# Performance work log

Hardware: AMD Instinct MI355X
Metric: run time of the kernel (lower is better)

## Reference

```python
import jax, jax.numpy as jnp
import numpy as np

B, E, H = 16384, 1024, 1024  # batch, input_size(=delta_size=mask_size), hidden_size


def setup_inputs() -> dict:
    key = jax.random.key(0)
    ks = jax.random.split(key, 16)
    stdv = 1.0 / np.sqrt(H)
    u = lambda k, shape: jax.random.uniform(k, shape, jnp.float32, -stdv, stdv)
    return {
        "x": jax.random.normal(ks[0], (B, E), jnp.float32),
        "x_mask": (jax.random.uniform(ks[1], (B, E)) < 0.5).astype(jnp.float32),
        "delta": jax.random.uniform(ks[2], (B, E), jnp.float32),
        "x_last_observed": jax.random.normal(ks[3], (B, E), jnp.float32),
        "x_mean": jax.random.normal(ks[4], (B, E), jnp.float32),
        "hs": jax.random.normal(ks[5], (B, H), jnp.float32),
        # gamma decay linears (delta_size -> delta_size), torch Linear convention y = x @ W.T + b
        "gx_w": u(ks[6], (E, E)), "gx_b": u(ks[7], (E,)),
        "gh_w": u(ks[8], (E, E)), "gh_b": u(ks[9], (E,)),
        # GRU cell (input 2E -> hidden H), gates ordered [r, z, n]
        "w_ih": u(ks[10], (2 * E, 3 * H)), "b_ih": u(ks[11], (3 * H,)),
        "w_hh": u(ks[12], (H, 3 * H)), "b_hh": u(ks[13], (3 * H,)),
    }


def reference(x, x_mask, delta, x_last_observed, x_mean, hs,
              gx_w, gx_b, gh_w, gh_b, w_ih, w_hh, b_ih, b_hh):
    # decay gates: exp(-max(0, Linear(delta)))
    delta_x = jnp.exp(-jax.nn.relu(delta @ gx_w.T + gx_b))  # [B, E]
    delta_h = jnp.exp(-jax.nn.relu(delta @ gh_w.T + gh_b))  # [B, H] (E == H)
    # masked blend of observed / decayed-last / mean
    x_t = x_mask * x + (1.0 - x_mask) * (delta_x * x_last_observed + (1.0 - delta_x) * x_mean)
    h = delta_h * hs
    inputs = jnp.concatenate([x_t, x_mask], axis=-1)  # [B, 2E]
    gi = inputs @ w_ih + b_ih                         # [B, 3H]
    gh = h @ w_hh + b_hh                              # [B, 3H]
    i_r, i_z, i_n = jnp.split(gi, 3, axis=-1)
    h_r, h_z, h_n = jnp.split(gh, 3, axis=-1)
    r = jax.nn.sigmoid(i_r + h_r)
    z = jax.nn.sigmoid(i_z + h_z)
    n = jnp.tanh(i_n + r * h_n)
    return (1.0 - z) * n + z * h
```

## Files before the change

### kernel.cpp

```cpp
#include <hip/hip_runtime.h>
#include <hip/hip_bf16.h>
#include <stdint.h>


#define Bn 16384
#define En 1024
#define Hn 1024

typedef __bf16 bf16x8 __attribute__((ext_vector_type(8)));
typedef float f32x4 __attribute__((ext_vector_type(4)));
typedef unsigned short u16x8 __attribute__((ext_vector_type(8)));

__device__ __forceinline__ void gload_lds16(const void* g, void* l) {
  __builtin_amdgcn_global_load_lds(
      (const __attribute__((address_space(1))) void*)g,
      (__attribute__((address_space(3))) void*)l, 16, 0, 0);
}

__device__ __forceinline__ unsigned short f2bf(float f) {
  __hip_bfloat16 h = __float2bfloat16(f);
  return __builtin_bit_cast(unsigned short, h);
}


__global__ void conv_f32_bf16(const float* __restrict__ in,
                              unsigned short* __restrict__ out, long n) {
  long stride = (long)gridDim.x * blockDim.x;
  for (long i = (long)blockIdx.x * blockDim.x + threadIdx.x; i * 8 < n; i += stride) {
    long b = i * 8;
    float4 a0 = *(const float4*)&in[b];
    float4 a1 = *(const float4*)&in[b + 4];
    u16x8 o;
    o[0] = f2bf(a0.x); o[1] = f2bf(a0.y); o[2] = f2bf(a0.z); o[3] = f2bf(a0.w);
    o[4] = f2bf(a1.x); o[5] = f2bf(a1.y); o[6] = f2bf(a1.z); o[7] = f2bf(a1.w);
    *(u16x8*)&out[b] = o;
  }
}

__global__ void conv_mask_k(const float* __restrict__ in,
                            unsigned short* __restrict__ U) {
  long n = (long)Bn * En;
  long stride = (long)gridDim.x * blockDim.x;
  for (long i = (long)blockIdx.x * blockDim.x + threadIdx.x; i * 8 < n; i += stride) {
    long b = i * 8;
    long row = b >> 10;
    int col = (int)(b & 1023);
    float4 a0 = *(const float4*)&in[b];
    float4 a1 = *(const float4*)&in[b + 4];
    u16x8 o;
    o[0] = f2bf(a0.x); o[1] = f2bf(a0.y); o[2] = f2bf(a0.z); o[3] = f2bf(a0.w);
    o[4] = f2bf(a1.x); o[5] = f2bf(a1.y); o[6] = f2bf(a1.z); o[7] = f2bf(a1.w);
    *(u16x8*)&U[row * 2048 + 1024 + col] = o;
  }
}

__global__ void transpose_conv(const float* __restrict__ in,
                               unsigned short* __restrict__ out, int R, int C) {
  __shared__ float tile[32][33];
  int bc = blockIdx.x * 32, br = blockIdx.y * 32;
  int tx = threadIdx.x, ty = threadIdx.y;
#pragma unroll
  for (int i = 0; i < 32; i += 8)
    tile[ty + i][tx] = in[(size_t)(br + ty + i) * C + (bc + tx)];
  __syncthreads();
#pragma unroll
  for (int i = 0; i < 32; i += 8)
    out[(size_t)(bc + ty + i) * R + (br + tx)] = f2bf(tile[tx][ty + i]);
}


template <int EPI>
__launch_bounds__(256)
__global__ void gemm_nt(const unsigned short* __restrict__ A,
                        const unsigned short* __restrict__ Bt,
                        int M, int N, int K,
                        const float* __restrict__ bias,
                        const float* __restrict__ e0, const float* __restrict__ e1,
                        const float* __restrict__ e2, const float* __restrict__ e3,
                        unsigned short* __restrict__ ob, float* __restrict__ of,
                        int ldo) {
  __shared__ unsigned short sA[128 * 32];
  __shared__ unsigned short sB[128 * 32];
  const int t = threadIdx.x;
  const int lane = t & 63;
  const int w = t >> 6;
  const int wr = w >> 1, wc = w & 1;
  const int rowA0 = blockIdx.x * 128, colB0 = blockIdx.y * 128;

  f32x4 acc[4][4] = {};

  const int fe0 = t * 8;
  const int r0 = fe0 >> 5, c0 = fe0 & 31;
  const int fe1 = (t + 256) * 8;
  const int r1 = fe1 >> 5, c1 = fe1 & 31;

  const unsigned short* Ab0 = A + (size_t)(rowA0 + r0) * K + c0;
  const unsigned short* Ab1 = A + (size_t)(rowA0 + r1) * K + c1;
  const unsigned short* Bb0 = Bt + (size_t)(colB0 + r0) * K + c0;
  const unsigned short* Bb1 = Bt + (size_t)(colB0 + r1) * K + c1;
  unsigned short* sA0 = &sA[t * 8];
  unsigned short* sA1 = &sA[(t + 256) * 8];
  unsigned short* sB0 = &sB[t * 8];
  unsigned short* sB1 = &sB[(t + 256) * 8];

  const int arow = lane & 15;
  const int kh = (lane >> 4) * 8;

  for (int k0 = 0; k0 < K; k0 += 32) {
    gload_lds16(Ab0 + k0, sA0);
    gload_lds16(Ab1 + k0, sA1);
    gload_lds16(Bb0 + k0, sB0);
    gload_lds16(Bb1 + k0, sB1);
    __syncthreads();
    bf16x8 af[4], bfr[4];
#pragma unroll
    for (int m = 0; m < 4; ++m)
      af[m] = *(const bf16x8*)&sA[(wr * 64 + m * 16 + arow) * 32 + kh];
#pragma unroll
    for (int n = 0; n < 4; ++n)
      bfr[n] = *(const bf16x8*)&sB[(wc * 64 + n * 16 + arow) * 32 + kh];
#pragma unroll
    for (int m = 0; m < 4; ++m)
#pragma unroll
      for (int n = 0; n < 4; ++n)
        acc[m][n] = __builtin_amdgcn_mfma_f32_16x16x32_bf16(af[m], bfr[n], acc[m][n], 0, 0, 0);
    __syncthreads();
  }

  const int crow0 = (lane >> 4) * 4;
  const int ccol = lane & 15;
#pragma unroll
  for (int m = 0; m < 4; ++m) {
#pragma unroll
    for (int n = 0; n < 4; ++n) {
#pragma unroll
      for (int j = 0; j < 4; ++j) {
        const int row = rowA0 + wr * 64 + m * 16 + crow0 + j;
        const int col = colB0 + wc * 64 + n * 16 + ccol;
        float v = acc[m][n][j];
        if constexpr (EPI == 0) {
          float dx = expf(-fmaxf(v + bias[col], 0.f));
          size_t idx = (size_t)row * 1024 + col;
          float xv = e0[idx], mv = e1[idx], xl = e2[idx], xm = e3[idx];
          float xt = mv * xv + (1.f - mv) * (dx * xl + (1.f - dx) * xm);
          ob[(size_t)row * ldo + col] = f2bf(xt);
        } else if constexpr (EPI == 1) {
          float dh = expf(-fmaxf(v + bias[col], 0.f));
          float hv = dh * e0[(size_t)row * 1024 + col];
          ob[(size_t)row * ldo + col] = f2bf(hv);
          of[(size_t)row * ldo + col] = hv;
        } else {
          of[(size_t)row * (size_t)ldo + col] = v;
        }
      }
    }
  }
}

__device__ __forceinline__ float sigm(float x) { return 1.f / (1.f + expf(-x)); }

__global__ void gates_k(const float* __restrict__ Gi, const float* __restrict__ Gh,
                        const float* Hf, const float* __restrict__ b_ih,
                        const float* __restrict__ b_hh, float* out,
                        int rows) {
  long n4 = (long)rows * Hn / 4;
  long stride = (long)gridDim.x * blockDim.x;
  for (long i4 = (long)blockIdx.x * blockDim.x + threadIdx.x; i4 < n4; i4 += stride) {
    long i = i4 * 4;
    long row = i >> 10;
    int col = (int)(i & 1023);
    const float* gi = Gi + row * 3072 + col;
    const float* gh = Gh + row * 3072 + col;
    float4 ir = *(const float4*)(gi);
    float4 iz = *(const float4*)(gi + 1024);
    float4 in_ = *(const float4*)(gi + 2048);
    float4 hr = *(const float4*)(gh);
    float4 hz = *(const float4*)(gh + 1024);
    float4 hn = *(const float4*)(gh + 2048);
    float4 bir = *(const float4*)&b_ih[col];
    float4 biz = *(const float4*)&b_ih[1024 + col];
    float4 bin_ = *(const float4*)&b_ih[2048 + col];
    float4 bhr = *(const float4*)&b_hh[col];
    float4 bhz = *(const float4*)&b_hh[1024 + col];
    float4 bhn = *(const float4*)&b_hh[2048 + col];
    float4 hv = *(const float4*)&Hf[i];
    float4 o;
#pragma unroll
    for (int c = 0; c < 4; ++c) {
      float r0 = sigm(((const float*)&ir)[c] + ((const float*)&bir)[c] +
                      ((const float*)&hr)[c] + ((const float*)&bhr)[c]);
      float z0 = sigm(((const float*)&iz)[c] + ((const float*)&biz)[c] +
                      ((const float*)&hz)[c] + ((const float*)&bhz)[c]);
      float nn = tanhf(((const float*)&in_)[c] + ((const float*)&bin_)[c] +
                       r0 * (((const float*)&hn)[c] + ((const float*)&bhn)[c]));
      ((float*)&o)[c] = (1.f - z0) * nn + z0 * ((const float*)&hv)[c];
    }
    *(float4*)&out[i] = o;
  }
}


extern "C" void kernel_launch(void* const* d_in, const int* in_sizes, int n_in,
                              void* d_out, int out_size, void* d_ws, size_t ws_size,
                              hipStream_t stream) {
  const float* x     = (const float*)d_in[0];
  const float* xmask = (const float*)d_in[1];
  const float* delta = (const float*)d_in[2];
  const float* xlast = (const float*)d_in[3];
  const float* xmean = (const float*)d_in[4];
  const float* hs    = (const float*)d_in[5];
  const float* gx_w  = (const float*)d_in[6];
  const float* gx_b  = (const float*)d_in[7];
  const float* gh_w  = (const float*)d_in[8];
  const float* gh_b  = (const float*)d_in[9];
  const float* w_ih  = (const float*)d_in[10];
  const float* b_ih  = (const float*)d_in[11];
  const float* w_hh  = (const float*)d_in[12];
  const float* b_hh  = (const float*)d_in[13];
  float* out = (float*)d_out;

  char* ws = (char*)d_ws;
  size_t off = 0;
  auto alloc = [&](size_t bytes) {
    char* p = ws + off;
    off += (bytes + 255) & ~(size_t)255;
    return p;
  };
  unsigned short* delta_bf = (unsigned short*)alloc((size_t)Bn * En * 2);
  unsigned short* U        = (unsigned short*)alloc((size_t)Bn * 2 * En * 2);
  unsigned short* Hbf      = (unsigned short*)alloc((size_t)Bn * Hn * 2);
  unsigned short* gxw_bf   = (unsigned short*)alloc((size_t)En * En * 2);
  unsigned short* ghw_bf   = (unsigned short*)alloc((size_t)En * En * 2);
  unsigned short* wihT     = (unsigned short*)alloc((size_t)3 * Hn * 2 * En * 2);
  unsigned short* whhT     = (unsigned short*)alloc((size_t)3 * Hn * Hn * 2);
  float*          Hf32     = out;

  int nchunk = 64;
  for (int c = 4; c <= 64; c *= 2) {
    size_t need = off + 2ull * (Bn / c) * 3 * Hn * 4 + 512;
    if (need <= ws_size) { nchunk = c; break; }
  }
  const int CROWS = Bn / nchunk;
  float* GiC = (float*)alloc((size_t)CROWS * 3 * Hn * 4);
  float* GhC = (float*)alloc((size_t)CROWS * 3 * Hn * 4);

  conv_f32_bf16<<<2048, 256, 0, stream>>>(delta, delta_bf, (long)Bn * En);
  conv_f32_bf16<<<512, 256, 0, stream>>>(gx_w, gxw_bf, (long)En * En);
  conv_f32_bf16<<<512, 256, 0, stream>>>(gh_w, ghw_bf, (long)En * En);
  conv_mask_k<<<2048, 256, 0, stream>>>(xmask, U);
  transpose_conv<<<dim3(3 * Hn / 32, 2 * En / 32), dim3(32, 8), 0, stream>>>(w_ih, wihT, 2 * En, 3 * Hn);
  transpose_conv<<<dim3(3 * Hn / 32, Hn / 32), dim3(32, 8), 0, stream>>>(w_hh, whhT, Hn, 3 * Hn);

  gemm_nt<0><<<dim3(Bn / 128, En / 128), 256, 0, stream>>>(
      delta_bf, gxw_bf, Bn, En, En, gx_b, x, xmask, xlast, xmean, U, nullptr, 2 * En);
  gemm_nt<1><<<dim3(Bn / 128, Hn / 128), 256, 0, stream>>>(
      delta_bf, ghw_bf, Bn, Hn, En, gh_b, hs, nullptr, nullptr, nullptr, Hbf, Hf32, Hn);

  for (int c = 0; c < nchunk; ++c) {
    const unsigned short* Uc = U + (size_t)c * CROWS * 2 * En;
    const unsigned short* Hc = Hbf + (size_t)c * CROWS * Hn;
    const float* Hfc = Hf32 + (size_t)c * CROWS * Hn;
    float* outc = out + (size_t)c * CROWS * Hn;
    gemm_nt<2><<<dim3(CROWS / 128, 3 * Hn / 128), 256, 0, stream>>>(
        Uc, wihT, CROWS, 3 * Hn, 2 * En, nullptr, nullptr, nullptr, nullptr, nullptr,
        nullptr, GiC, 3 * Hn);
    gemm_nt<2><<<dim3(CROWS / 128, 3 * Hn / 128), 256, 0, stream>>>(
        Hc, whhT, CROWS, 3 * Hn, Hn, nullptr, nullptr, nullptr, nullptr, nullptr,
        nullptr, GhC, 3 * Hn);
    gates_k<<<2048, 256, 0, stream>>>(GiC, GhC, Hfc, b_ih, b_hh, outc, CROWS);
  }
}
```

Before: 1.149 ms.

## Stage GEMM epilogue through LDS for vectorized stores and remap blocks per XCD

The GEMM epilogue now writes each wave's accumulator fragment to a shared-memory staging buffer, then reads it back row-contiguously so bias, auxiliary inputs and outputs use float4 and 4-wide bf16 accesses instead of scalar strided ones. The 2D grid is also flattened to 1D and remapped so consecutive tiles land on the same XCD, which should improve L2 reuse of A/B tiles. The cost is extra LDS (about 19KB per block), which may lower occupancy, plus some index arithmetic.

```diff
diff --git a/kernel.cpp b/kernel.cpp
--- a/kernel.cpp
+++ b/kernel.cpp
@@ -10,6 +10,7 @@
 typedef __bf16 bf16x8 __attribute__((ext_vector_type(8)));
 typedef float f32x4 __attribute__((ext_vector_type(4)));
 typedef unsigned short u16x8 __attribute__((ext_vector_type(8)));
+typedef unsigned short u16x4 __attribute__((ext_vector_type(4)));
 
 __device__ __forceinline__ void gload_lds16(const void* g, void* l) {
   __builtin_amdgcn_global_load_lds(
@@ -73,7 +74,7 @@
 __launch_bounds__(256)
 __global__ void gemm_nt(const unsigned short* __restrict__ A,
                         const unsigned short* __restrict__ Bt,
-                        int M, int N, int K,
+                        int gridX, int gridY, int K,
                         const float* __restrict__ bias,
                         const float* __restrict__ e0, const float* __restrict__ e1,
                         const float* __restrict__ e2, const float* __restrict__ e3,
@@ -81,23 +82,32 @@
                         int ldo) {
   __shared__ unsigned short sA[128 * 32];
   __shared__ unsigned short sB[128 * 32];
+  __shared__ float sEpi[4][16][76];
+
+  const int nwg = gridX * gridY;
+  const int q = nwg >> 3, r = nwg & 7;
+  const int xcd = (int)blockIdx.x & 7, pos = (int)blockIdx.x >> 3;
+  const int wg = (xcd < r ? xcd * (q + 1) : r * (q + 1) + (xcd - r) * q) + pos;
+  const int by = wg / gridX;
+  const int bx = wg - by * gridX;
+
   const int t = threadIdx.x;
   const int lane = t & 63;
   const int w = t >> 6;
   const int wr = w >> 1, wc = w & 1;
-  const int rowA0 = blockIdx.x * 128, colB0 = blockIdx.y * 128;
+  const int rowA0 = bx * 128, colB0 = by * 128;
 
   f32x4 acc[4][4] = {};
 
   const int fe0 = t * 8;
-  const int r0 = fe0 >> 5, c0 = fe0 & 31;
+  const int r0 = fe0 >> 5, c0e = fe0 & 31;
   const int fe1 = (t + 256) * 8;
-  const int r1 = fe1 >> 5, c1 = fe1 & 31;
-
-  const unsigned short* Ab0 = A + (size_t)(rowA0 + r0) * K + c0;
-  const unsigned short* Ab1 = A + (size_t)(rowA0 + r1) * K + c1;
-  const unsigned short* Bb0 = Bt + (size_t)(colB0 + r0) * K + c0;
-  const unsigned short* Bb1 = Bt + (size_t)(colB0 + r1) * K + c1;
+  const int r1 = fe1 >> 5, c1e = fe1 & 31;
+
+  const unsigned short* Ab0 = A + (size_t)(rowA0 + r0) * K + c0e;
+  const unsigned short* Ab1 = A + (size_t)(rowA0 + r1) * K + c1e;
+  const unsigned short* Bb0 = Bt + (size_t)(colB0 + r0) * K + c0e;
+  const unsigned short* Bb1 = Bt + (size_t)(colB0 + r1) * K + c1e;
   unsigned short* sA0 = &sA[t * 8];
   unsigned short* sA1 = &sA[(t + 256) * 8];
   unsigned short* sB0 = &sB[t * 8];
@@ -127,31 +137,59 @@
     __syncthreads();
   }
 
+  const int ccol = lane & 15;
   const int crow0 = (lane >> 4) * 4;
-  const int ccol = lane & 15;
+  const int rr0 = lane >> 4;
+  const int cc0 = (lane & 15) * 4;
+
 #pragma unroll
   for (int m = 0; m < 4; ++m) {
 #pragma unroll
-    for (int n = 0; n < 4; ++n) {
-#pragma unroll
-      for (int j = 0; j < 4; ++j) {
-        const int row = rowA0 + wr * 64 + m * 16 + crow0 + j;
-        const int col = colB0 + wc * 64 + n * 16 + ccol;
-        float v = acc[m][n][j];
-        if constexpr (EPI == 0) {
-          float dx = expf(-fmaxf(v + bias[col], 0.f));
-          size_t idx = (size_t)row * 1024 + col;
-          float xv = e0[idx], mv = e1[idx], xl = e2[idx], xm = e3[idx];
-          float xt = mv * xv + (1.f - mv) * (dx * xl + (1.f - dx) * xm);
-          ob[(size_t)row * ldo + col] = f2bf(xt);
-        } else if constexpr (EPI == 1) {
-          float dh = expf(-fmaxf(v + bias[col], 0.f));
-          float hv = dh * e0[(size_t)row * 1024 + col];
-          ob[(size_t)row * ldo + col] = f2bf(hv);
-          of[(size_t)row * ldo + col] = hv;
-        } else {
-          of[(size_t)row * (size_t)ldo + col] = v;
+    for (int n = 0; n < 4; ++n)
+#pragma unroll
+      for (int j = 0; j < 4; ++j)
+        sEpi[w][crow0 + j][n * 16 + ccol] = acc[m][n][j];
+#pragma unroll
+    for (int v = 0; v < 4; ++v) {
+      const int rr = v * 4 + rr0;
+      const int grow = rowA0 + wr * 64 + m * 16 + rr;
+      const int gcol = colB0 + wc * 64 + cc0;
+      float4 vv = *(const float4*)&sEpi[w][rr][cc0];
+      const float* vp = (const float*)&vv;
+      if constexpr (EPI == 0) {
+        float4 bi = *(const float4*)&bias[gcol];
+        size_t idx = (size_t)grow * 1024 + gcol;
+        float4 xv = *(const float4*)&e0[idx];
+        float4 mv = *(const float4*)&e1[idx];
+        float4 xl = *(const float4*)&e2[idx];
+        float4 xm = *(const float4*)&e3[idx];
+        u16x4 o;
+#pragma unroll
+        for (int c = 0; c < 4; ++c) {
+          float dx = expf(-fmaxf(vp[c] + ((const float*)&bi)[c], 0.f));
+          float xvv = ((const float*)&xv)[c], mvv = ((const float*)&mv)[c];
+          float xlv = ((const float*)&xl)[c], xmv = ((const float*)&xm)[c];
+          float xt = mvv * xvv + (1.f - mvv) * (dx * xlv + (1.f - dx) * xmv);
+          o[c] = f2bf(xt);
         }
+        *(u16x4*)&ob[(size_t)grow * ldo + gcol] = o;
+      } else if constexpr (EPI == 1) {
+        float4 bi = *(const float4*)&bias[gcol];
+        size_t idx = (size_t)grow * 1024 + gcol;
+        float4 hv = *(const float4*)&e0[idx];
+        u16x4 o;
+        float4 of4;
+#pragma unroll
+        for (int c = 0; c < 4; ++c) {
+          float dh = expf(-fmaxf(vp[c] + ((const float*)&bi)[c], 0.f));
+          float hval = dh * ((const float*)&hv)[c];
+          o[c] = f2bf(hval);
+          ((float*)&of4)[c] = hval;
+        }
+        *(u16x4*)&ob[(size_t)grow * ldo + gcol] = o;
+        *(float4*)&of[(size_t)grow * ldo + gcol] = of4;
+      } else {
+        *(float4*)&of[(size_t)grow * (size_t)ldo + gcol] = vv;
       }
     }
   }
@@ -251,22 +289,24 @@
   transpose_conv<<<dim3(3 * Hn / 32, 2 * En / 32), dim3(32, 8), 0, stream>>>(w_ih, wihT, 2 * En, 3 * Hn);
   transpose_conv<<<dim3(3 * Hn / 32, Hn / 32), dim3(32, 8), 0, stream>>>(w_hh, whhT, Hn, 3 * Hn);
 
-  gemm_nt<0><<<dim3(Bn / 128, En / 128), 256, 0, stream>>>(
-      delta_bf, gxw_bf, Bn, En, En, gx_b, x, xmask, xlast, xmean, U, nullptr, 2 * En);
-  gemm_nt<1><<<dim3(Bn / 128, Hn / 128), 256, 0, stream>>>(
-      delta_bf, ghw_bf, Bn, Hn, En, gh_b, hs, nullptr, nullptr, nullptr, Hbf, Hf32, Hn);
+  gemm_nt<0><<<Bn / 128 * (En / 128), 256, 0, stream>>>(
+      delta_bf, gxw_bf, Bn / 128, En / 128, En, gx_b, x, xmask, xlast, xmean, U,
+      nullptr, 2 * En);
+  gemm_nt<1><<<Bn / 128 * (Hn / 128), 256, 0, stream>>>(
+      delta_bf, ghw_bf, Bn / 128, Hn / 128, En, gh_b, hs, nullptr, nullptr, nullptr,
+      Hbf, Hf32, Hn);
 
   for (int c = 0; c < nchunk; ++c) {
     const unsigned short* Uc = U + (size_t)c * CROWS * 2 * En;
     const unsigned short* Hc = Hbf + (size_t)c * CROWS * Hn;
     const float* Hfc = Hf32 + (size_t)c * CROWS * Hn;
     float* outc = out + (size_t)c * CROWS * Hn;
-    gemm_nt<2><<<dim3(CROWS / 128, 3 * Hn / 128), 256, 0, stream>>>(
-        Uc, wihT, CROWS, 3 * Hn, 2 * En, nullptr, nullptr, nullptr, nullptr, nullptr,
-        nullptr, GiC, 3 * Hn);
-    gemm_nt<2><<<dim3(CROWS / 128, 3 * Hn / 128), 256, 0, stream>>>(
-        Hc, whhT, CROWS, 3 * Hn, Hn, nullptr, nullptr, nullptr, nullptr, nullptr,
-        nullptr, GhC, 3 * Hn);
+    gemm_nt<2><<<CROWS / 128 * (3 * Hn / 128), 256, 0, stream>>>(
+        Uc, wihT, CROWS / 128, 3 * Hn / 128, 2 * En, nullptr, nullptr, nullptr,
+        nullptr, nullptr, nullptr, GiC, 3 * Hn);
+    gemm_nt<2><<<CROWS / 128 * (3 * Hn / 128), 256, 0, stream>>>(
+        Hc, whhT, CROWS / 128, 3 * Hn / 128, Hn, nullptr, nullptr, nullptr,
+        nullptr, nullptr, nullptr, GhC, 3 * Hn);
     gates_k<<<2048, 256, 0, stream>>>(GiC, GhC, Hfc, b_ih, b_hh, outc, CROWS);
   }
 }
```

Result: no change. 1.159 ms (+0.9%).
